# Kernel optimization log

Measured on AMD Instinct MI355X. Metric: run time of the kernel, lower is better.

The kernel has to match this reference:

```python
import jax, jax.numpy as jnp
import numpy as np

N, E, K, F_IN, H = 50000, 640000, 3, 128, 128


def setup_inputs() -> dict:
    key = jax.random.key(0)
    ks = jax.random.split(key, 14)
    s = 0.05
    return {
        "x": jax.random.normal(ks[0], (N, F_IN), jnp.float32),
        "edge_index": jax.random.randint(ks[1], (2, E), 0, N, dtype=jnp.int32),
        "edge_weight": jax.random.uniform(ks[2], (E,), jnp.float32, minval=0.1, maxval=1.0),
        "W_x": jax.random.normal(ks[3], (4, F_IN, H), jnp.float32) * s,   # dense input weights (i,f,c,o)
        "w_c": jax.random.normal(ks[4], (3, H), jnp.float32) * s,         # peephole weights (i,f,o)
        "b": jax.random.normal(ks[5], (4, H), jnp.float32) * s,           # gate biases (i,f,c,o)
        "theta": jax.random.normal(ks[6], (4, K, H, H), jnp.float32) * s, # ChebConv weights per gate
        "theta_b": jax.random.normal(ks[7], (4, H), jnp.float32) * s,     # ChebConv biases per gate
        "gcn_w": jax.random.normal(ks[8], (H, H), jnp.float32) * s,
        "gcn_b": jnp.zeros((H,), jnp.float32),
        "bn_gamma": jnp.ones((H,), jnp.float32),
        "bn_beta": jnp.zeros((H,), jnp.float32),
        "bn_mean": jax.random.normal(ks[9], (H,), jnp.float32) * 0.1,
        "bn_var": jax.random.uniform(ks[10], (H,), jnp.float32, minval=0.5, maxval=1.5),
        "lin_w": jax.random.normal(ks[11], (H, 1), jnp.float32) * s,
        "lin_b": jnp.zeros((1,), jnp.float32),
    }


def reference(x, edge_index, edge_weight, W_x, w_c, b, theta, theta_b, gcn_w, gcn_b, bn_gamma, bn_beta, bn_mean, bn_var, lin_w, lin_b):
    n = x.shape[0]
    src, dst = edge_index[0], edge_index[1]

    # --- ChebConv normalization (sym, lambda_max=2): L_hat = -D^{-1/2} A D^{-1/2}, zero diagonal ---
    deg = jnp.zeros((n,), x.dtype).at[src].add(edge_weight)
    safe = jnp.where(deg > 0, deg, 1.0)
    dis = jnp.where(deg > 0, jax.lax.rsqrt(safe), 0.0)
    lw = -dis[src] * edge_weight * dis[dst]  # per-edge scaled-Laplacian weight

    def prop(h):  # out[i] = sum_{edges j->i} lw * h[j]
        return jnp.zeros_like(h).at[dst].add(lw[:, None] * h[src])

    def cheb(h, th, tb):  # sum_k T_k(L_hat) h @ theta_k + bias, Chebyshev recurrence
        Tx0, out = h, h @ th[0]
        Tx1 = prop(h)
        out = out + Tx1 @ th[1]
        for k in range(2, K):
            Tx2 = 2.0 * prop(Tx1) - Tx0
            out = out + Tx2 @ th[k]
            Tx0, Tx1 = Tx1, Tx2
        return out + tb

    # --- GCLSTM with H = C = 0 (module passes no initial state) ---
    Hs = jnp.zeros((n, W_x.shape[2]), x.dtype)
    Cs = jnp.zeros_like(Hs)
    I = jax.nn.sigmoid(x @ W_x[0] + cheb(Hs, theta[0], theta_b[0]) + w_c[0] * Cs + b[0])
    Fg = jax.nn.sigmoid(x @ W_x[1] + cheb(Hs, theta[1], theta_b[1]) + w_c[1] * Cs + b[1])
    T = jnp.tanh(x @ W_x[2] + cheb(Hs, theta[2], theta_b[2]) + b[2])
    Cs = Fg * Cs + I * T
    O = jax.nn.sigmoid(x @ W_x[3] + cheb(Hs, theta[3], theta_b[3]) + w_c[2] * Cs + b[3])
    Hs = O * jnp.tanh(Cs)

    # --- GCNConv(H) with unit edge weights + added self-loops ---
    h = Hs @ gcn_w
    deg_g = jnp.ones((n,), x.dtype).at[dst].add(jnp.ones((edge_index.shape[1],), x.dtype))
    dg = jax.lax.rsqrt(deg_g)
    g = jnp.zeros_like(h).at[dst].add((dg[src] * dg[dst])[:, None] * h[src]) + (dg * dg)[:, None] * h + gcn_b

    g = jax.nn.relu(g)
    g = bn_gamma * (g - bn_mean) * jax.lax.rsqrt(bn_var + 1e-5) + bn_beta  # BatchNorm1d (eval)
    return g @ lin_w + lin_b  # Dropout = identity in eval
```

## Files before the change

### kernel.cpp

```cpp
#include <hip/hip_runtime.h>
#include <hip/hip_bf16.h>

#define NN 50000
#define NE 640000
#define CAP 64
#define NGB 782
#define NBIN 782
#define NA 196
#define EPA 3328
#define ORow 784

typedef unsigned short ushort_t;
typedef unsigned int uint_t;
typedef __attribute__((ext_vector_type(8))) short bf16x8;
typedef __attribute__((ext_vector_type(4))) float f32x4;

__device__ __forceinline__ float b2f(ushort_t u) {
    union { uint_t u; float f; } v; v.u = ((uint_t)u) << 16; return v.f;
}
__device__ __forceinline__ ushort_t f2b(float f) {
    union { float f; uint_t u; } v; v.f = f;
    uint_t u = v.u;
    uint_t r = u + 0x7fffu + ((u >> 16) & 1u);
    return (ushort_t)(r >> 16);
}
__device__ __forceinline__ float fsig(float x)  { return __builtin_amdgcn_rcpf(1.0f + __expf(-x)); }
__device__ __forceinline__ float ftanh(float x) { return 1.0f - 2.0f * __builtin_amdgcn_rcpf(1.0f + __expf(2.0f * x)); }
__device__ __forceinline__ float ldm(const void* p, int i, int mf) {
    return mf ? ((const float*)p)[i] : b2f(((const ushort_t*)p)[i]);
}

#define OFF_HB    0
#define OFF_CHUNK 12800000
#define OFF_OFFS  15409152
#define OFF_CNT   16023808
#define OFF_WT    16223808
#define OFF_COEF  16354880
#define OFF_MODE  16357444
#define WS_REQ    16357448

__global__ void fb_k(ushort_t* __restrict__ out, int n) {
    int i = blockIdx.x * blockDim.x + threadIdx.x;
    if (i < n) out[i] = 0;
}

__launch_bounds__(256)
__global__ void bsprep_k(const ushort_t* __restrict__ x, const int* __restrict__ ei,
                         const void* __restrict__ Wx, const void* __restrict__ gcnw,
                         const void* __restrict__ wc, const void* __restrict__ bb,
                         const void* __restrict__ thb,
                         const void* __restrict__ gam, const void* __restrict__ bet,
                         const void* __restrict__ mea, const void* __restrict__ var,
                         const void* __restrict__ linw, const void* __restrict__ linb,
                         ushort_t* __restrict__ WT, float* __restrict__ coef,
                         int* __restrict__ mode,
                         uint_t* __restrict__ chunk, int* __restrict__ offs) {
    __shared__ int sh[1280];
    __shared__ float red[128];
    int b = blockIdx.x, t = threadIdx.x;

    if (b < NA) {
        int a = b;
        int e0 = a * EPA; if (e0 > NE) e0 = NE;
        int e1 = e0 + EPA; if (e1 > NE) e1 = NE;
        const int* dstp = ei + NE;
        for (int i = t; i < NBIN; i += 256) sh[i] = 0;
        __syncthreads();
        for (int i = e0 + t; i < e1; i += 256) atomicAdd(&sh[dstp[i] >> 6], 1);
        __syncthreads();
        int b0 = t * 4;
        int s = 0;
        #pragma unroll
        for (int j = 0; j < 4; j++) { int bi = b0 + j; if (bi < NBIN) s += sh[bi]; }
        sh[1024 + t] = s;
        __syncthreads();
        for (int off = 1; off < 256; off <<= 1) {
            int v = (t >= off) ? sh[1024 + t - off] : 0;
            __syncthreads();
            sh[1024 + t] += v;
            __syncthreads();
        }
        int run = (t == 0) ? 0 : sh[1024 + t - 1];
        int* orow = offs + a * ORow;
        #pragma unroll
        for (int j = 0; j < 4; j++) {
            int bi = b0 + j;
            if (bi < NBIN) {
                int c = sh[bi];
                orow[bi] = run;
                sh[bi] = run;
                run += c;
            }
        }
        if (t == 0) orow[NBIN] = e1 - e0;
        __syncthreads();
        uint_t* ck = chunk + a * EPA;
        for (int i = e0 + t; i < e1; i += 256) {
            int d = dstp[i], sn = ei[i];
            int pos = atomicAdd(&sh[d >> 6], 1);
            ck[pos] = ((uint_t)sn << 6) | (uint_t)(d & 63);
        }
        return;
    }

    int bad = 0;
    for (int i = t; i < 4096; i += 256) {
        int e = (x[i] >> 7) & 0xFF;
        if (e >= 0xC0) bad++;
    }
    sh[t] = bad; __syncthreads();
    for (int o = 128; o >= 1; o >>= 1) { if (t < o) sh[t] += sh[t + o]; __syncthreads(); }
    int mf = (sh[0] > 8) ? 1 : 0;

    int wb = b - NA;
    if (wb < 32) {
        int gid = wb * 256 + t;
        int m  = gid >> 11;
        int u  = gid & 2047;
        int k  = u >> 4;
        int f0 = (u & 15) << 3;
        const int srcoff[4] = { 0, 2 * 16384, 3 * 16384, 0 };
        const void* S = (m == 3) ? gcnw : Wx;
        int sbase = srcoff[m] + k * 128 + f0;
        ushort_t vals[8];
        if (mf == 0) {
            bf16x8 v = *(const bf16x8*)((const ushort_t*)S + sbase);
            #pragma unroll
            for (int i = 0; i < 8; i++) vals[i] = (ushort_t)v[i];
        } else {
            const float* Sf = (const float*)S + sbase;
            #pragma unroll
            for (int i = 0; i < 8; i++) vals[i] = f2b(Sf[i]);
        }
        ushort_t* D = WT + m * 16384 + k;
        #pragma unroll
        for (int i = 0; i < 8; i++) D[(f0 + i) * 128] = vals[i];
    } else {
        if (t < 128) {
            float rs = rsqrtf(ldm(var, t, mf) + 1e-5f);
            float ga = ldm(gam, t, mf);
            float lw = ldm(linw, t, mf);
            coef[t]       = ldm(thb, t, mf)           + ldm(bb, t, mf);
            coef[128 + t] = ldm(thb, 2 * 128 + t, mf) + ldm(bb, 2 * 128 + t, mf);
            coef[256 + t] = ldm(thb, 3 * 128 + t, mf) + ldm(bb, 3 * 128 + t, mf);
            coef[384 + t] = ldm(wc, 2 * 128 + t, mf);
            coef[512 + t] = ga * rs * lw;
            red[t] = (ldm(bet, t, mf) - ldm(mea, t, mf) * ga * rs) * lw;
        }
        __syncthreads();
        for (int off = 64; off >= 1; off >>= 1) {
            if (t < off && t < 128) red[t] += red[t + off];
            __syncthreads();
        }
        if (t == 0) {
            coef[640] = red[0] + ldm(linb, 0, mf);
            mode[0] = mf;
        }
    }
}

__launch_bounds__(256)
__global__ void gacnt_k(const void* __restrict__ x, const ushort_t* __restrict__ WT,
                        const float* __restrict__ coef, const int* __restrict__ mode,
                        ushort_t* __restrict__ hb,
                        const uint_t* __restrict__ chunk, const int* __restrict__ offs,
                        int* __restrict__ cnt) {
    __shared__ __align__(16) char smem[17408];
    int b = blockIdx.x, t = threadIdx.x;

    if (b & 1) {
        int bin = b >> 1;
        int* P      = (int*)smem;
        int* sstart = (int*)(smem + 1024);
        int* lcnt   = (int*)(smem + 1808);
        if (t < 64) lcnt[t] = 0;
        int len = 0;
        if (t < NA) {
            int st = offs[t * ORow + bin];
            int en = offs[t * ORow + bin + 1];
            sstart[t] = st;
            len = en - st;
        }
        P[t] = len;
        __syncthreads();
        for (int off = 1; off < 256; off <<= 1) {
            int v = (t >= off) ? P[t - off] : 0;
            __syncthreads();
            P[t] += v;
            __syncthreads();
        }
        int T = P[255];
        for (int i = t; i < T; i += 256) {
            int lo = 0, hi = NA - 1;
            while (lo < hi) { int mid = (lo + hi) >> 1; if (P[mid] > i) hi = mid; else lo = mid + 1; }
            int prev = (lo == 0) ? 0 : P[lo - 1];
            uint_t w = chunk[lo * EPA + sstart[lo] + (i - prev)];
            atomicAdd(&lcnt[(int)(w & 63u)], 1);
        }
        __syncthreads();
        if (t < 64) { int node = (bin << 6) + t; if (node < NN) cnt[node] = lcnt[t]; }
        return;
    }

    ushort_t* tile = (ushort_t*)smem;
    int gb = b >> 1;
    int base = gb * 64;
    int mf = mode[0];

    for (int i = 0; i < 4; i++) {
        int idx = (i * 256 + t) * 8;
        int row = idx >> 7, col = idx & 127;
        int n = base + row;
        bf16x8 v;
        if (n >= NN) {
            v = (bf16x8)0;
        } else if (mf == 0) {
            v = *(const bf16x8*)((const ushort_t*)x + n * 128 + col);
        } else {
            const float* xf = (const float*)x + n * 128 + col;
            float4 lo = *(const float4*)xf;
            float4 hi = *(const float4*)(xf + 4);
            v[0] = (short)f2b(lo.x); v[1] = (short)f2b(lo.y);
            v[2] = (short)f2b(lo.z); v[3] = (short)f2b(lo.w);
            v[4] = (short)f2b(hi.x); v[5] = (short)f2b(hi.y);
            v[6] = (short)f2b(hi.z); v[7] = (short)f2b(hi.w);
        }
        *(bf16x8*)&tile[row * 136 + col] = v;
    }
    __syncthreads();

    int lane = t & 63, wave = t >> 6;
    int m = lane & 15, quad = lane >> 4;

    bf16x8 a[4][4];
    #pragma unroll
    for (int rt = 0; rt < 4; rt++)
        #pragma unroll
        for (int kt = 0; kt < 4; kt++)
            a[rt][kt] = *(const bf16x8*)&tile[(rt * 16 + m) * 136 + kt * 32 + quad * 8];
    __syncthreads();

    const ushort_t* WTi = WT;
    const ushort_t* WTc = WT + 16384;
    const ushort_t* WTo = WT + 2 * 16384;

    #pragma unroll
    for (int ft = 0; ft < 2; ft++) {
        int f = wave * 32 + ft * 16 + m;
        bf16x8 bi[4], bc[4], bo[4];
        #pragma unroll
        for (int kt = 0; kt < 4; kt++) {
            int off = f * 128 + kt * 32 + quad * 8;
            bi[kt] = *(const bf16x8*)(WTi + off);
            bc[kt] = *(const bf16x8*)(WTc + off);
            bo[kt] = *(const bf16x8*)(WTo + off);
        }
        float bi_f = coef[f], bc_f = coef[128 + f], bo_f = coef[256 + f], w2 = coef[384 + f];
        #pragma unroll
        for (int rt = 0; rt < 4; rt++) {
            f32x4 ai = {0,0,0,0}, ac = {0,0,0,0}, ao = {0,0,0,0};
            #pragma unroll
            for (int kt = 0; kt < 4; kt++) {
                ai = __builtin_amdgcn_mfma_f32_16x16x32_bf16(a[rt][kt], bi[kt], ai, 0, 0, 0);
                ac = __builtin_amdgcn_mfma_f32_16x16x32_bf16(a[rt][kt], bc[kt], ac, 0, 0, 0);
                ao = __builtin_amdgcn_mfma_f32_16x16x32_bf16(a[rt][kt], bo[kt], ao, 0, 0, 0);
            }
            #pragma unroll
            for (int r = 0; r < 4; r++) {
                float I  = fsig(ai[r] + bi_f);
                float T  = ftanh(ac[r] + bc_f);
                float Cs = I * T;
                float O  = fsig(ao[r] + w2 * Cs + bo_f);
                float Hs = O * ftanh(Cs);
                tile[(rt * 16 + quad * 4 + r) * 136 + f] = f2b(Hs);
            }
        }
    }
    __syncthreads();

    const ushort_t* WTg = WT + 3 * 16384;
    bf16x8 ah[4][4];
    #pragma unroll
    for (int rt = 0; rt < 4; rt++)
        #pragma unroll
        for (int kt = 0; kt < 4; kt++)
            ah[rt][kt] = *(const bf16x8*)&tile[(rt * 16 + m) * 136 + kt * 32 + quad * 8];

    #pragma unroll
    for (int ft = 0; ft < 2; ft++) {
        int f = wave * 32 + ft * 16 + m;
        bf16x8 bg[4];
        #pragma unroll
        for (int kt = 0; kt < 4; kt++)
            bg[kt] = *(const bf16x8*)(WTg + f * 128 + kt * 32 + quad * 8);
        #pragma unroll
        for (int rt = 0; rt < 4; rt++) {
            f32x4 acc = {0,0,0,0};
            #pragma unroll
            for (int kt = 0; kt < 4; kt++)
                acc = __builtin_amdgcn_mfma_f32_16x16x32_bf16(ah[rt][kt], bg[kt], acc, 0, 0, 0);
            #pragma unroll
            for (int r = 0; r < 4; r++) {
                int n = base + rt * 16 + quad * 4 + r;
                if (n < NN) hb[n * 128 + f] = f2b(acc[r]);
            }
        }
    }
}

__launch_bounds__(256)
__global__ void sgat_k(const uint_t* __restrict__ chunk, const int* __restrict__ offs,
                       const ushort_t* __restrict__ hb, const int* __restrict__ cnt,
                       const void* __restrict__ gcnb, const float* __restrict__ coef,
                       const int* __restrict__ mode, void* __restrict__ out) {
    __shared__ __align__(16) char smem[18448];
    int* P      = (int*)smem;
    int* sstart = (int*)(smem + 1024);
    int* lcnt   = (int*)(smem + 1808);
    uint_t* lbuck = (uint_t*)(smem + 2064);
    int b = blockIdx.x, t = threadIdx.x;
    int node0 = b << 6;

    if (t < 64) lcnt[t] = 0;
    int len = 0;
    if (t < NA) {
        int st = offs[t * ORow + b];
        int en = offs[t * ORow + b + 1];
        sstart[t] = st;
        len = en - st;
    }
    P[t] = len;
    __syncthreads();
    for (int off = 1; off < 256; off <<= 1) {
        int v = (t >= off) ? P[t - off] : 0;
        __syncthreads();
        P[t] += v;
        __syncthreads();
    }
    int T = P[255];
    for (int i = t; i < T; i += 256) {
        int lo = 0, hi = NA - 1;
        while (lo < hi) { int mid = (lo + hi) >> 1; if (P[mid] > i) hi = mid; else lo = mid + 1; }
        int prev = (lo == 0) ? 0 : P[lo - 1];
        uint_t w = chunk[lo * EPA + sstart[lo] + (i - prev)];
        int d6 = (int)(w & 63u);
        int sn = (int)(w >> 6);
        int p = atomicAdd(&lcnt[d6], 1);
        if (p < CAP) lbuck[(d6 << 6) + p] = (uint_t)sn;
    }
    __syncthreads();

    int mf = mode[0];
    int wave = t >> 6, lane = t & 63;
    int half = lane >> 5, sl = lane & 31;
    for (int q = 0; q < 16; q++) {
        int local = wave * 16 + q;
        int wid = node0 + local;
        if (wid >= NN) break;
        int c = lcnt[local];
        int deg = (c < CAP) ? c : CAP;
        const uint_t* lb = lbuck + (local << 6);
        float a0 = 0.0f, a1 = 0.0f, a2 = 0.0f, a3 = 0.0f;
        for (int j = half; j < deg; j += 4) {
            int ok2 = (j + 2 < deg);
            int s0 = (int)lb[j];
            int s1 = (int)lb[ok2 ? j + 2 : j];
            int cs0 = cnt[s0];
            int cs1 = cnt[s1];
            uint2 r0 = *(const uint2*)(hb + s0 * 128 + sl * 4);
            uint2 r1 = *(const uint2*)(hb + s1 * 128 + sl * 4);
            float w0 = rsqrtf(1.0f + (float)cs0);
            float w1 = ok2 ? rsqrtf(1.0f + (float)cs1) : 0.0f;
            a0 += w0 * b2f((ushort_t)(r0.x & 0xffffu)) + w1 * b2f((ushort_t)(r1.x & 0xffffu));
            a1 += w0 * b2f((ushort_t)(r0.x >> 16))     + w1 * b2f((ushort_t)(r1.x >> 16));
            a2 += w0 * b2f((ushort_t)(r0.y & 0xffffu)) + w1 * b2f((ushort_t)(r1.y & 0xffffu));
            a3 += w0 * b2f((ushort_t)(r0.y >> 16))     + w1 * b2f((ushort_t)(r1.y >> 16));
        }
        float d = rsqrtf(1.0f + (float)c);
        if (half == 0) {
            uint2 r = *(const uint2*)(hb + wid * 128 + sl * 4);
            a0 += d * b2f((ushort_t)(r.x & 0xffffu));
            a1 += d * b2f((ushort_t)(r.x >> 16));
            a2 += d * b2f((ushort_t)(r.y & 0xffffu));
            a3 += d * b2f((ushort_t)(r.y >> 16));
        }
        a0 += __shfl_xor(a0, 32); a1 += __shfl_xor(a1, 32);
        a2 += __shfl_xor(a2, 32); a3 += __shfl_xor(a3, 32);
        int fb = sl * 4;
        float g0 = d * a0 + ldm(gcnb, fb,     mf);
        float g1 = d * a1 + ldm(gcnb, fb + 1, mf);
        float g2 = d * a2 + ldm(gcnb, fb + 2, mf);
        float g3 = d * a3 + ldm(gcnb, fb + 3, mf);
        float v = fmaxf(g0, 0.0f) * coef[512 + fb]
                + fmaxf(g1, 0.0f) * coef[512 + fb + 1]
                + fmaxf(g2, 0.0f) * coef[512 + fb + 2]
                + fmaxf(g3, 0.0f) * coef[512 + fb + 3];
        #pragma unroll
        for (int o = 32; o >= 1; o >>= 1) v += __shfl_down(v, o);
        if (lane == 0) {
            float r = 0.5f * v + coef[640];
            if (mf) ((float*)out)[wid] = r;
            else    ((ushort_t*)out)[wid] = f2b(r);
        }
    }
}

extern "C" void kernel_launch(void* const* d_in, const int* in_sizes, int n_in,
                              void* d_out, int out_size, void* d_ws, size_t ws_size,
                              hipStream_t stream) {
    if (ws_size < (size_t)WS_REQ) {
        fb_k<<<(out_size + 255) / 256, 256, 0, stream>>>((ushort_t*)d_out, out_size);
        return;
    }
    const ushort_t* x = (const ushort_t*)d_in[0];
    const int*  ei   = (const int*)d_in[1];
    const void* Wx   = d_in[3];
    const void* wc   = d_in[4];
    const void* bb   = d_in[5];
    const void* thb  = d_in[7];
    const void* gcnw = d_in[8];
    const void* gcnb = d_in[9];
    const void* gam  = d_in[10];
    const void* bet  = d_in[11];
    const void* mea  = d_in[12];
    const void* var  = d_in[13];
    const void* linw = d_in[14];
    const void* linb = d_in[15];

    char* ws = (char*)d_ws;
    ushort_t* hb    = (ushort_t*)(ws + OFF_HB);
    uint_t*   chunk = (uint_t*)  (ws + OFF_CHUNK);
    int*      offs  = (int*)     (ws + OFF_OFFS);
    int*      cnt   = (int*)     (ws + OFF_CNT);
    ushort_t* WT    = (ushort_t*)(ws + OFF_WT);
    float*    coef  = (float*)   (ws + OFF_COEF);
    int*      mode  = (int*)     (ws + OFF_MODE);

    bsprep_k<<<NA + 33, 256, 0, stream>>>(x, ei, Wx, gcnw, wc, bb, thb,
                                          gam, bet, mea, var, linw, linb,
                                          WT, coef, mode, chunk, offs);
    gacnt_k<<<2 * NGB, 256, 0, stream>>>(x, WT, coef, mode, hb, chunk, offs, cnt);
    sgat_k<<<NBIN, 256, 0, stream>>>(chunk, offs, hb, cnt, gcnb, coef, mode, d_out);
}
```

Before: 203.1 us.

## Move neighbor bucketing into count kernel and gather via per-node CSR rows

The per-bin edge bucketing that sgat_k used to redo is now done once in the odd blocks of the middle kernel, which already scanned the chunk. Those blocks write a fixed-capacity per-node source list (bsrc, 64 slots per node) to global memory. The final kernel becomes a flat one-wave-per-node gather that reads this list, with four neighbor loads in flight per iteration instead of two. In exchange it writes and reads an extra 12.8 MB buffer and grows the workspace requirement, but removes the scan, binary search and shared-memory atomics from the last kernel and gives it more parallel waves.

```diff
diff --git a/kernel.cpp b/kernel.cpp
--- a/kernel.cpp
+++ b/kernel.cpp
@@ -31,13 +31,14 @@
 }
 
 #define OFF_HB    0
-#define OFF_CHUNK 12800000
-#define OFF_OFFS  15409152
-#define OFF_CNT   16023808
-#define OFF_WT    16223808
-#define OFF_COEF  16354880
-#define OFF_MODE  16357444
-#define WS_REQ    16357448
+#define OFF_BSRC  12800000
+#define OFF_CHUNK 25600000
+#define OFF_OFFS  28209152
+#define OFF_CNT   28823808
+#define OFF_WT    29023808
+#define OFF_COEF  29154880
+#define OFF_MODE  29157444
+#define WS_REQ    29157448
 
 __global__ void fb_k(ushort_t* __restrict__ out, int n) {
     int i = blockIdx.x * blockDim.x + threadIdx.x;
@@ -160,20 +161,23 @@
 }
 
 __launch_bounds__(256)
-__global__ void gacnt_k(const void* __restrict__ x, const ushort_t* __restrict__ WT,
-                        const float* __restrict__ coef, const int* __restrict__ mode,
-                        ushort_t* __restrict__ hb,
-                        const uint_t* __restrict__ chunk, const int* __restrict__ offs,
-                        int* __restrict__ cnt) {
-    __shared__ __align__(16) char smem[17408];
+__global__ void gasc_k(const void* __restrict__ x, const ushort_t* __restrict__ WT,
+                       const float* __restrict__ coef, const int* __restrict__ mode,
+                       ushort_t* __restrict__ hb,
+                       const uint_t* __restrict__ chunk, const int* __restrict__ offs,
+                       int* __restrict__ bsrc, int* __restrict__ cnt) {
+    __shared__ __align__(16) char smem[18448];
     int b = blockIdx.x, t = threadIdx.x;
 
     if (b & 1) {
         int bin = b >> 1;
+        int node0 = bin << 6;
         int* P      = (int*)smem;
         int* sstart = (int*)(smem + 1024);
         int* lcnt   = (int*)(smem + 1808);
+        uint_t* lbuck = (uint_t*)(smem + 2064);
         if (t < 64) lcnt[t] = 0;
+        for (int i = t; i < 64 * CAP; i += 256) lbuck[i] = 0;
         int len = 0;
         if (t < NA) {
             int st = offs[t * ORow + bin];
@@ -195,10 +199,19 @@
             while (lo < hi) { int mid = (lo + hi) >> 1; if (P[mid] > i) hi = mid; else lo = mid + 1; }
             int prev = (lo == 0) ? 0 : P[lo - 1];
             uint_t w = chunk[lo * EPA + sstart[lo] + (i - prev)];
-            atomicAdd(&lcnt[(int)(w & 63u)], 1);
-        }
-        __syncthreads();
-        if (t < 64) { int node = (bin << 6) + t; if (node < NN) cnt[node] = lcnt[t]; }
+            int d6 = (int)(w & 63u);
+            int sn = (int)(w >> 6);
+            int p = atomicAdd(&lcnt[d6], 1);
+            if (p < CAP) lbuck[(d6 << 6) + p] = (uint_t)sn;
+        }
+        __syncthreads();
+        if (t < 64) { int node = node0 + t; if (node < NN) cnt[node] = lcnt[t]; }
+        const int4* lb4 = (const int4*)lbuck;
+        int4* bs4 = (int4*)bsrc;
+        for (int i = t; i < 1024; i += 256) {
+            int node = node0 + (i >> 4);
+            if (node < NN) bs4[(node0 << 4) + i] = lb4[i];
+        }
         return;
     }
 
@@ -309,99 +322,69 @@
 }
 
 __launch_bounds__(256)
-__global__ void sgat_k(const uint_t* __restrict__ chunk, const int* __restrict__ offs,
-                       const ushort_t* __restrict__ hb, const int* __restrict__ cnt,
-                       const void* __restrict__ gcnb, const float* __restrict__ coef,
-                       const int* __restrict__ mode, void* __restrict__ out) {
-    __shared__ __align__(16) char smem[18448];
-    int* P      = (int*)smem;
-    int* sstart = (int*)(smem + 1024);
-    int* lcnt   = (int*)(smem + 1808);
-    uint_t* lbuck = (uint_t*)(smem + 2064);
-    int b = blockIdx.x, t = threadIdx.x;
-    int node0 = b << 6;
-
-    if (t < 64) lcnt[t] = 0;
-    int len = 0;
-    if (t < NA) {
-        int st = offs[t * ORow + b];
-        int en = offs[t * ORow + b + 1];
-        sstart[t] = st;
-        len = en - st;
-    }
-    P[t] = len;
-    __syncthreads();
-    for (int off = 1; off < 256; off <<= 1) {
-        int v = (t >= off) ? P[t - off] : 0;
-        __syncthreads();
-        P[t] += v;
-        __syncthreads();
-    }
-    int T = P[255];
-    for (int i = t; i < T; i += 256) {
-        int lo = 0, hi = NA - 1;
-        while (lo < hi) { int mid = (lo + hi) >> 1; if (P[mid] > i) hi = mid; else lo = mid + 1; }
-        int prev = (lo == 0) ? 0 : P[lo - 1];
-        uint_t w = chunk[lo * EPA + sstart[lo] + (i - prev)];
-        int d6 = (int)(w & 63u);
-        int sn = (int)(w >> 6);
-        int p = atomicAdd(&lcnt[d6], 1);
-        if (p < CAP) lbuck[(d6 << 6) + p] = (uint_t)sn;
-    }
-    __syncthreads();
-
+__global__ void gat_out_k(const ushort_t* __restrict__ hb, const int* __restrict__ cnt,
+                          const int* __restrict__ bsrc,
+                          const void* __restrict__ gcnb, const float* __restrict__ coef,
+                          const int* __restrict__ mode, void* __restrict__ out) {
+    int wid  = (blockIdx.x * blockDim.x + threadIdx.x) >> 6;
+    int lane = threadIdx.x & 63;
+    if (wid >= NN) return;
+    int half = lane >> 5, sl = lane & 31;
+    int c = cnt[wid]; if (c < 0) c = 0;
+    int deg = (c < CAP) ? c : CAP;
+    const int* brow = bsrc + wid * CAP;
+
+    float a0 = 0.0f, a1 = 0.0f, a2 = 0.0f, a3 = 0.0f;
+    for (int j = half; j < deg; j += 8) {
+        int i1 = j + 2, i2 = j + 4, i3 = j + 6;
+        int s0 = brow[j];
+        int s1 = brow[i1 & (CAP - 1)];
+        int s2 = brow[i2 & (CAP - 1)];
+        int s3 = brow[i3 & (CAP - 1)];
+        int c0 = cnt[s0], c1 = cnt[s1], c2 = cnt[s2], c3 = cnt[s3];
+        uint2 r0 = *(const uint2*)(hb + s0 * 128 + sl * 4);
+        uint2 r1 = *(const uint2*)(hb + s1 * 128 + sl * 4);
+        uint2 r2 = *(const uint2*)(hb + s2 * 128 + sl * 4);
+        uint2 r3 = *(const uint2*)(hb + s3 * 128 + sl * 4);
+        float w0 = rsqrtf(1.0f + (float)c0);
+        float w1 = (i1 < deg) ? rsqrtf(1.0f + (float)c1) : 0.0f;
+        float w2 = (i2 < deg) ? rsqrtf(1.0f + (float)c2) : 0.0f;
+        float w3 = (i3 < deg) ? rsqrtf(1.0f + (float)c3) : 0.0f;
+        a0 += w0 * b2f((ushort_t)(r0.x & 0xffffu)) + w1 * b2f((ushort_t)(r1.x & 0xffffu))
+            + w2 * b2f((ushort_t)(r2.x & 0xffffu)) + w3 * b2f((ushort_t)(r3.x & 0xffffu));
+        a1 += w0 * b2f((ushort_t)(r0.x >> 16))     + w1 * b2f((ushort_t)(r1.x >> 16))
+            + w2 * b2f((ushort_t)(r2.x >> 16))     + w3 * b2f((ushort_t)(r3.x >> 16));
+        a2 += w0 * b2f((ushort_t)(r0.y & 0xffffu)) + w1 * b2f((ushort_t)(r1.y & 0xffffu))
+            + w2 * b2f((ushort_t)(r2.y & 0xffffu)) + w3 * b2f((ushort_t)(r3.y & 0xffffu));
+        a3 += w0 * b2f((ushort_t)(r0.y >> 16))     + w1 * b2f((ushort_t)(r1.y >> 16))
+            + w2 * b2f((ushort_t)(r2.y >> 16))     + w3 * b2f((ushort_t)(r3.y >> 16));
+    }
+    float d = rsqrtf(1.0f + (float)c);
+    if (half == 0) {
+        uint2 r = *(const uint2*)(hb + wid * 128 + sl * 4);
+        a0 += d * b2f((ushort_t)(r.x & 0xffffu));
+        a1 += d * b2f((ushort_t)(r.x >> 16));
+        a2 += d * b2f((ushort_t)(r.y & 0xffffu));
+        a3 += d * b2f((ushort_t)(r.y >> 16));
+    }
+    a0 += __shfl_xor(a0, 32); a1 += __shfl_xor(a1, 32);
+    a2 += __shfl_xor(a2, 32); a3 += __shfl_xor(a3, 32);
     int mf = mode[0];
-    int wave = t >> 6, lane = t & 63;
-    int half = lane >> 5, sl = lane & 31;
-    for (int q = 0; q < 16; q++) {
-        int local = wave * 16 + q;
-        int wid = node0 + local;
-        if (wid >= NN) break;
-        int c = lcnt[local];
-        int deg = (c < CAP) ? c : CAP;
-        const uint_t* lb = lbuck + (local << 6);
-        float a0 = 0.0f, a1 = 0.0f, a2 = 0.0f, a3 = 0.0f;
-        for (int j = half; j < deg; j += 4) {
-            int ok2 = (j + 2 < deg);
-            int s0 = (int)lb[j];
-            int s1 = (int)lb[ok2 ? j + 2 : j];
-            int cs0 = cnt[s0];
-            int cs1 = cnt[s1];
-            uint2 r0 = *(const uint2*)(hb + s0 * 128 + sl * 4);
-            uint2 r1 = *(const uint2*)(hb + s1 * 128 + sl * 4);
-            float w0 = rsqrtf(1.0f + (float)cs0);
-            float w1 = ok2 ? rsqrtf(1.0f + (float)cs1) : 0.0f;
-            a0 += w0 * b2f((ushort_t)(r0.x & 0xffffu)) + w1 * b2f((ushort_t)(r1.x & 0xffffu));
-            a1 += w0 * b2f((ushort_t)(r0.x >> 16))     + w1 * b2f((ushort_t)(r1.x >> 16));
-            a2 += w0 * b2f((ushort_t)(r0.y & 0xffffu)) + w1 * b2f((ushort_t)(r1.y & 0xffffu));
-            a3 += w0 * b2f((ushort_t)(r0.y >> 16))     + w1 * b2f((ushort_t)(r1.y >> 16));
-        }
-        float d = rsqrtf(1.0f + (float)c);
-        if (half == 0) {
-            uint2 r = *(const uint2*)(hb + wid * 128 + sl * 4);
-            a0 += d * b2f((ushort_t)(r.x & 0xffffu));
-            a1 += d * b2f((ushort_t)(r.x >> 16));
-            a2 += d * b2f((ushort_t)(r.y & 0xffffu));
-            a3 += d * b2f((ushort_t)(r.y >> 16));
-        }
-        a0 += __shfl_xor(a0, 32); a1 += __shfl_xor(a1, 32);
-        a2 += __shfl_xor(a2, 32); a3 += __shfl_xor(a3, 32);
-        int fb = sl * 4;
-        float g0 = d * a0 + ldm(gcnb, fb,     mf);
-        float g1 = d * a1 + ldm(gcnb, fb + 1, mf);
-        float g2 = d * a2 + ldm(gcnb, fb + 2, mf);
-        float g3 = d * a3 + ldm(gcnb, fb + 3, mf);
-        float v = fmaxf(g0, 0.0f) * coef[512 + fb]
-                + fmaxf(g1, 0.0f) * coef[512 + fb + 1]
-                + fmaxf(g2, 0.0f) * coef[512 + fb + 2]
-                + fmaxf(g3, 0.0f) * coef[512 + fb + 3];
-        #pragma unroll
-        for (int o = 32; o >= 1; o >>= 1) v += __shfl_down(v, o);
-        if (lane == 0) {
-            float r = 0.5f * v + coef[640];
-            if (mf) ((float*)out)[wid] = r;
-            else    ((ushort_t*)out)[wid] = f2b(r);
-        }
+    int fb = sl * 4;
+    float g0 = d * a0 + ldm(gcnb, fb,     mf);
+    float g1 = d * a1 + ldm(gcnb, fb + 1, mf);
+    float g2 = d * a2 + ldm(gcnb, fb + 2, mf);
+    float g3 = d * a3 + ldm(gcnb, fb + 3, mf);
+    float v = fmaxf(g0, 0.0f) * coef[512 + fb]
+            + fmaxf(g1, 0.0f) * coef[512 + fb + 1]
+            + fmaxf(g2, 0.0f) * coef[512 + fb + 2]
+            + fmaxf(g3, 0.0f) * coef[512 + fb + 3];
+    #pragma unroll
+    for (int o = 32; o >= 1; o >>= 1) v += __shfl_down(v, o);
+    if (lane == 0) {
+        float r = 0.5f * v + coef[640];
+        if (mf) ((float*)out)[wid] = r;
+        else    ((ushort_t*)out)[wid] = f2b(r);
     }
 }
 
@@ -429,6 +412,7 @@
 
     char* ws = (char*)d_ws;
     ushort_t* hb    = (ushort_t*)(ws + OFF_HB);
+    int*      bsrc  = (int*)     (ws + OFF_BSRC);
     uint_t*   chunk = (uint_t*)  (ws + OFF_CHUNK);
     int*      offs  = (int*)     (ws + OFF_OFFS);
     int*      cnt   = (int*)     (ws + OFF_CNT);
@@ -439,6 +423,6 @@
     bsprep_k<<<NA + 33, 256, 0, stream>>>(x, ei, Wx, gcnw, wc, bb, thb,
                                           gam, bet, mea, var, linw, linb,
                                           WT, coef, mode, chunk, offs);
-    gacnt_k<<<2 * NGB, 256, 0, stream>>>(x, WT, coef, mode, hb, chunk, offs, cnt);
-    sgat_k<<<NBIN, 256, 0, stream>>>(chunk, offs, hb, cnt, gcnb, coef, mode, d_out);
-}
+    gasc_k<<<2 * NGB, 256, 0, stream>>>(x, WT, coef, mode, hb, chunk, offs, bsrc, cnt);
+    gat_out_k<<<(NN * 64 + 255) / 256, 256, 0, stream>>>(hb, cnt, bsrc, gcnb, coef, mode, d_out);
+}
```

Result: faster. 182.1 us (-10.3%).
